# Kernel tuning notes

Measured on AMD Instinct MI355X. Metric: run time of the kernel, lower is better.

Reference implementation:

```python
import jax, jax.numpy as jnp
import numpy as np
from jax.scipy.special import logsumexp

T, B, D, L = 1024, 32, 768, 48
NEG = jnp.float32(-1e20)


def setup_inputs() -> dict:
    key = jax.random.key(0)
    ks = jax.random.split(key, 10)
    feats = jax.random.normal(ks[0], (T, B, D), jnp.float32)
    # tags: True = label disallowed at this position (partial annotation mask)
    tags = jax.random.uniform(ks[1], (T, B, L)) < 0.3
    lens = jax.random.randint(ks[2], (B,), T // 2, T + 1)
    W = jax.random.normal(ks[3], (D, L), jnp.float32) * 0.02
    b = jnp.zeros((L,), jnp.float32)
    base = jnp.float32(1.0 / L)
    begin_transition = jnp.full((L,), base) + 0.01 * jax.random.normal(ks[4], (L,), jnp.float32)
    transitions = jnp.full((L, L), base) + 0.01 * jax.random.normal(ks[5], (L, L), jnp.float32)
    end_transition = jnp.full((L,), base) + 0.01 * jax.random.normal(ks[6], (L,), jnp.float32)
    begin_constraints = jax.random.uniform(ks[7], (L,)) < 0.2
    end_constraints = jax.random.uniform(ks[8], (L,)) < 0.2
    transition_constraints = jax.random.uniform(ks[9], (L, L)) < 0.2
    return {
        "feats": feats, "tags": tags, "lens": lens,
        "W": W, "b": b,
        "begin_transition": begin_transition, "transitions": transitions,
        "end_transition": end_transition,
        "begin_constraints": begin_constraints, "end_constraints": end_constraints,
        "transition_constraints": transition_constraints,
    }


def _crf_logZ(emissions, begin, trans, end, tag_mask, lens):
    """Forward algorithm over [T,B,L] emissions; tag_mask True = disallowed.
    Returns log partition per batch element, read out at step lens-1."""
    fs0 = emissions[0] + begin[None, :]              # [B, L]
    fs0 = jnp.where(tag_mask[0], NEG, fs0)

    def step(prev, xs):
        em_t, m_t = xs
        # new[b, j] = logsumexp_k(prev[b, k] + trans[j, k]) + em_t[b, j]
        new = logsumexp(prev[:, None, :] + trans[None, :, :], axis=-1) + em_t
        new = jnp.where(m_t, NEG, new)
        return new, new

    _, ys = jax.lax.scan(step, fs0, (emissions[1:], tag_mask[1:]))
    all_fs = jnp.concatenate([fs0[None], ys], axis=0)        # [T, B, L]
    last = all_fs[lens - 1, jnp.arange(lens.shape[0])]       # [B, L]
    return logsumexp(last + end[None, :], axis=-1)           # [B]


def reference(feats, tags, lens, W, b, begin_transition, transitions,
              end_transition, begin_constraints, end_constraints,
              transition_constraints):
    # feature2labels (Dropout is identity in eval)
    emissions = jnp.einsum('tbd,dl->tbl', feats, W) + b      # [T, B, L]
    no_mask = jnp.zeros_like(tags)

    # forward_alg: unconstrained partition function
    fwd = _crf_logZ(emissions, begin_transition, transitions,
                    end_transition, no_mask, lens)

    # partial_score: constrained params + gold tag masking
    begin_m = jnp.where(begin_constraints, NEG, begin_transition)
    trans_m = jnp.where(transition_constraints, NEG, transitions)
    end_m = jnp.where(end_constraints, NEG, end_transition)
    par = _crf_logZ(emissions, begin_m, trans_m, end_m, tags, lens)

    # criterion per batch element (sum over batch = original scalar loss)
    return fwd - par                                          # [B]
```

## Files before the change

### kernel.cpp

```cpp
#include <hip/hip_runtime.h>

#define T_ 1024
#define B_ 32
#define D_ 768
#define L_ 48
#define TB_ (T_ * B_)

__global__ __launch_bounds__(256, 1) void emis_gemm(
    const float* __restrict__ feats, const float* __restrict__ W,
    const float* __restrict__ bias, float* __restrict__ E) {
  __shared__ float fbuf[128 * 64];
  __shared__ float wbuf[48 * 68];
  const int tid = threadIdx.x;
  const int wv = tid >> 6;
  const int lane = tid & 63;
  const int cg = tid & 7;
  const int rg = tid >> 3;
  const int c0 = cg * 6;
  const int rowbase = blockIdx.x * 128;
  const int r7 = rg & 7;

  float acc[4][6];
#pragma unroll
  for (int i = 0; i < 4; i++)
#pragma unroll
    for (int c = 0; c < 6; c++) acc[i][c] = 0.f;

  for (int kc = 0; kc < D_; kc += 64) {
    __syncthreads();

#pragma unroll
    for (int inst = 0; inst < 8; inst++) {
      const int rowstart = wv * 32 + inst * 4;
      const int r = rowstart + (lane >> 4);
      const int slot = lane & 15;
      const int gch = slot ^ (r & 7);
      const float* g = feats + (size_t)(rowbase + r) * D_ + kc + gch * 4;
      float* l = fbuf + rowstart * 64;
      __builtin_amdgcn_global_load_lds(
          (const __attribute__((address_space(1))) uint32_t*)g,
          (__attribute__((address_space(3))) uint32_t*)l, 16, 0, 0);
    }

#pragma unroll
    for (int i = 0; i < 12; i++) {
      const int idx = tid + i * 256;
      const int ko = idx / 48;
      const int j = idx - ko * 48;
      wbuf[j * 68 + ko] = W[(kc + ko) * L_ + j];
    }

    __syncthreads();

#pragma unroll 4
    for (int k4 = 0; k4 < 16; k4++) {
      float4 fv[4];
      float4 wv4[6];
      const int sch = (k4 ^ r7) << 2;
#pragma unroll
      for (int i = 0; i < 4; i++)
        fv[i] = *(const float4*)(fbuf + (rg + 32 * i) * 64 + sch);
#pragma unroll
      for (int c = 0; c < 6; c++)
        wv4[c] = *(const float4*)(wbuf + (c0 + c) * 68 + k4 * 4);
#pragma unroll
      for (int i = 0; i < 4; i++) {
#pragma unroll
        for (int c = 0; c < 6; c++) {
          acc[i][c] = fmaf(fv[i].x, wv4[c].x, acc[i][c]);
          acc[i][c] = fmaf(fv[i].y, wv4[c].y, acc[i][c]);
          acc[i][c] = fmaf(fv[i].z, wv4[c].z, acc[i][c]);
          acc[i][c] = fmaf(fv[i].w, wv4[c].w, acc[i][c]);
        }
      }
    }
  }

#pragma unroll
  for (int i = 0; i < 4; i++) {
    float* dst = E + (size_t)(rowbase + rg + 32 * i) * L_ + c0;
#pragma unroll
    for (int c = 0; c < 6; c += 2) {
      float2 v;
      v.x = __expf(acc[i][c + 0] + bias[c0 + c + 0]);
      v.y = __expf(acc[i][c + 1] + bias[c0 + c + 1]);
      *(float2*)(dst + c) = v;
    }
  }
}

__global__ __launch_bounds__(64, 1) void crf_scan(
    const float* __restrict__ E, const int* __restrict__ tags,
    const int* __restrict__ lens, const float* __restrict__ begin,
    const float* __restrict__ trans, const float* __restrict__ endt,
    const int* __restrict__ bc, const int* __restrict__ ec,
    const int* __restrict__ tc, float* __restrict__ out) {
  const int s = blockIdx.x;
  const int pass = s & 1;
  const int b = s >> 1;
  const int lane = threadIdx.x;
  const bool act = lane < L_;
  const int len = lens[b];
  const int stride = B_ * L_;
  const int base = b * L_ + (act ? lane : 0);

  float P[L_];
#pragma unroll
  for (int k = 0; k < L_; k++) P[k] = 0.f;
  if (act) {
#pragma unroll
    for (int k = 0; k < L_; k++) {
      float p = __expf(trans[lane * L_ + k]);
      if (pass && tc[lane * L_ + k]) p = 0.f;
      P[k] = p;
    }
  }

  float a = 0.f;
  if (act) {
    a = E[base] * __expf(begin[lane]);
    if (pass && (bc[lane] || tags[base])) a = 0.f;
  }
  float logacc = 0.f;

  auto step = [&](float ev, int tg, bool rescale) {
    const int ai = __float_as_int(a);
    int sa[L_];
#pragma unroll
    for (int k = 0; k < L_; k++) sa[k] = __builtin_amdgcn_readlane(ai, k);
    float s0 = 0.f, s1 = 0.f, s2 = 0.f, s3 = 0.f;
#pragma unroll
    for (int k = 0; k < L_; k += 4) {
      s0 = fmaf(__int_as_float(sa[k + 0]), P[k + 0], s0);
      s1 = fmaf(__int_as_float(sa[k + 1]), P[k + 1], s1);
      s2 = fmaf(__int_as_float(sa[k + 2]), P[k + 2], s2);
      s3 = fmaf(__int_as_float(sa[k + 3]), P[k + 3], s3);
    }
    float u = ((s0 + s1) + (s2 + s3)) * ev;
    if (pass && tg) u = 0.f;
    if (rescale) {
      float m = u;
#pragma unroll
      for (int off = 32; off; off >>= 1) m = fmaxf(m, __shfl_xor(m, off, 64));
      m = fmaxf(m, 1e-30f);
      u = u / m;
      logacc += __logf(m);
    }
    a = u;
  };

  float e8[8];
  int tg8[8];
#pragma unroll
  for (int i = 0; i < 8; i++) {
    e8[i] = E[(1 + i) * stride + base];
    tg8[i] = pass ? tags[(1 + i) * stride + base] : 0;
  }

  int t = 1;
  for (; t + 8 <= len; t += 8) {
    float p8[8];
    int q8[8];
#pragma unroll
    for (int i = 0; i < 8; i++) {
      int tt = t + 8 + i;
      tt = (tt < len) ? tt : (len - 1);
      p8[i] = E[tt * stride + base];
      q8[i] = pass ? tags[tt * stride + base] : 0;
    }
#pragma unroll
    for (int i = 0; i < 8; i++) step(e8[i], tg8[i], i == 7);
#pragma unroll
    for (int i = 0; i < 8; i++) { e8[i] = p8[i]; tg8[i] = q8[i]; }
  }
#pragma unroll
  for (int i = 0; i < 8; i++) {
    if (t + i < len) step(e8[i], tg8[i], false);
  }

  float z = 0.f;
  if (act) {
    float ez = __expf(endt[lane]);
    if (pass && ec[lane]) ez = 0.f;
    z = a * ez;
  }
#pragma unroll
  for (int off = 32; off; off >>= 1) z += __shfl_xor(z, off, 64);
  const float logZ = logacc + __logf(z);
  if (lane == 0) atomicAdd(out + b, pass ? -logZ : logZ);
}

extern "C" void kernel_launch(void* const* d_in, const int* in_sizes, int n_in,
                              void* d_out, int out_size, void* d_ws,
                              size_t ws_size, hipStream_t stream) {
  (void)in_sizes; (void)n_in; (void)out_size; (void)ws_size;
  const float* feats = (const float*)d_in[0];
  const int* tags = (const int*)d_in[1];
  const int* lens = (const int*)d_in[2];
  const float* W = (const float*)d_in[3];
  const float* bias = (const float*)d_in[4];
  const float* begin = (const float*)d_in[5];
  const float* trans = (const float*)d_in[6];
  const float* endt = (const float*)d_in[7];
  const int* bc = (const int*)d_in[8];
  const int* ec = (const int*)d_in[9];
  const int* tc = (const int*)d_in[10];

  float* E = (float*)d_ws;
  float* out = (float*)d_out;

  hipMemsetAsync(d_out, 0, B_ * sizeof(float), stream);

  emis_gemm<<<dim3(TB_ / 128), dim3(256), 0, stream>>>(feats, W, bias, E);
  crf_scan<<<dim3(2 * B_), dim3(64), 0, stream>>>(E, tags, lens, begin, trans,
                                                  endt, bc, ec, tc, out);
}
```

Before: 448.3 us.

## Double-buffer GEMM staging and pack CRF scan chains into multi-wave blocks

The emission GEMM now double-buffers the feature and weight tiles in shared memory, prefetching the next K-chunk while computing the current one, so there is one barrier per chunk instead of two. The CRF scan folds the tag mask into the emission value at load time, replaces the division with a hardware reciprocal, and packs eight sequence chains into each 512-thread block instead of one 64-thread block per chain. Packing chains onto fewer CUs may make the latency-bound scan waves compete for issue slots. The extra shared buffer also raises LDS use in the GEMM.

New measurement: 837.8 us. +86.9%, slower.

```diff
diff --git a/kernel.cpp b/kernel.cpp
--- a/kernel.cpp
+++ b/kernel.cpp
@@ -9,8 +9,8 @@
 __global__ __launch_bounds__(256, 1) void emis_gemm(
     const float* __restrict__ feats, const float* __restrict__ W,
     const float* __restrict__ bias, float* __restrict__ E) {
-  __shared__ float fbuf[128 * 64];
-  __shared__ float wbuf[48 * 68];
+  __shared__ float fbuf[2][128 * 64];
+  __shared__ float wbuf[2][48 * 68];
   const int tid = threadIdx.x;
   const int wv = tid >> 6;
   const int lane = tid & 63;
@@ -26,9 +26,9 @@
 #pragma unroll
     for (int c = 0; c < 6; c++) acc[i][c] = 0.f;
 
-  for (int kc = 0; kc < D_; kc += 64) {
-    __syncthreads();
-
+  float wreg[12];
+
+  auto stage_feats = [&](int kc, int bufi) {
 #pragma unroll
     for (int inst = 0; inst < 8; inst++) {
       const int rowstart = wv * 32 + inst * 4;
@@ -36,22 +36,42 @@
       const int slot = lane & 15;
       const int gch = slot ^ (r & 7);
       const float* g = feats + (size_t)(rowbase + r) * D_ + kc + gch * 4;
-      float* l = fbuf + rowstart * 64;
+      float* l = &fbuf[bufi][rowstart * 64];
       __builtin_amdgcn_global_load_lds(
           (const __attribute__((address_space(1))) uint32_t*)g,
           (__attribute__((address_space(3))) uint32_t*)l, 16, 0, 0);
     }
-
+  };
+  auto load_w = [&](int kc) {
 #pragma unroll
     for (int i = 0; i < 12; i++) {
       const int idx = tid + i * 256;
       const int ko = idx / 48;
       const int j = idx - ko * 48;
-      wbuf[j * 68 + ko] = W[(kc + ko) * L_ + j];
-    }
-
-    __syncthreads();
-
+      wreg[i] = W[(kc + ko) * L_ + j];
+    }
+  };
+  auto store_w = [&](int bufi) {
+#pragma unroll
+    for (int i = 0; i < 12; i++) {
+      const int idx = tid + i * 256;
+      const int ko = idx / 48;
+      const int j = idx - ko * 48;
+      wbuf[bufi][j * 68 + ko] = wreg[i];
+    }
+  };
+
+  stage_feats(0, 0);
+  load_w(0);
+  store_w(0);
+  __syncthreads();
+
+  for (int c = 0; c < 12; c++) {
+    const int cur = c & 1, nxt = cur ^ 1;
+    if (c + 1 < 12) {
+      stage_feats((c + 1) * 64, nxt);
+      load_w((c + 1) * 64);
+    }
 #pragma unroll 4
     for (int k4 = 0; k4 < 16; k4++) {
       float4 fv[4];
@@ -59,21 +79,23 @@
       const int sch = (k4 ^ r7) << 2;
 #pragma unroll
       for (int i = 0; i < 4; i++)
-        fv[i] = *(const float4*)(fbuf + (rg + 32 * i) * 64 + sch);
-#pragma unroll
-      for (int c = 0; c < 6; c++)
-        wv4[c] = *(const float4*)(wbuf + (c0 + c) * 68 + k4 * 4);
+        fv[i] = *(const float4*)(&fbuf[cur][(rg + 32 * i) * 64 + sch]);
+#pragma unroll
+      for (int cc = 0; cc < 6; cc++)
+        wv4[cc] = *(const float4*)(&wbuf[cur][(c0 + cc) * 68 + k4 * 4]);
 #pragma unroll
       for (int i = 0; i < 4; i++) {
 #pragma unroll
-        for (int c = 0; c < 6; c++) {
-          acc[i][c] = fmaf(fv[i].x, wv4[c].x, acc[i][c]);
-          acc[i][c] = fmaf(fv[i].y, wv4[c].y, acc[i][c]);
-          acc[i][c] = fmaf(fv[i].z, wv4[c].z, acc[i][c]);
-          acc[i][c] = fmaf(fv[i].w, wv4[c].w, acc[i][c]);
+        for (int cc = 0; cc < 6; cc++) {
+          acc[i][cc] = fmaf(fv[i].x, wv4[cc].x, acc[i][cc]);
+          acc[i][cc] = fmaf(fv[i].y, wv4[cc].y, acc[i][cc]);
+          acc[i][cc] = fmaf(fv[i].z, wv4[cc].z, acc[i][cc]);
+          acc[i][cc] = fmaf(fv[i].w, wv4[cc].w, acc[i][cc]);
         }
       }
     }
+    if (c + 1 < 12) store_w(nxt);
+    __syncthreads();
   }
 
 #pragma unroll
@@ -89,16 +111,17 @@
   }
 }
 
-__global__ __launch_bounds__(64, 1) void crf_scan(
+__global__ __launch_bounds__(512, 2) void crf_scan(
     const float* __restrict__ E, const int* __restrict__ tags,
     const int* __restrict__ lens, const float* __restrict__ begin,
     const float* __restrict__ trans, const float* __restrict__ endt,
     const int* __restrict__ bc, const int* __restrict__ ec,
     const int* __restrict__ tc, float* __restrict__ out) {
-  const int s = blockIdx.x;
+  const int wvid = threadIdx.x >> 6;
+  const int lane = threadIdx.x & 63;
+  const int s = blockIdx.x * 8 + wvid;
   const int pass = s & 1;
   const int b = s >> 1;
-  const int lane = threadIdx.x;
   const bool act = lane < L_;
   const int len = lens[b];
   const int stride = B_ * L_;
@@ -123,7 +146,13 @@
   }
   float logacc = 0.f;
 
-  auto step = [&](float ev, int tg, bool rescale) {
+  auto ldE = [&](int tt) -> float {
+    float v = E[tt * stride + base];
+    if (pass && tags[tt * stride + base]) v = 0.f;
+    return v;
+  };
+
+  auto step = [&](float ev, bool rescale) {
     const int ai = __float_as_int(a);
     int sa[L_];
 #pragma unroll
@@ -137,45 +166,38 @@
       s3 = fmaf(__int_as_float(sa[k + 3]), P[k + 3], s3);
     }
     float u = ((s0 + s1) + (s2 + s3)) * ev;
-    if (pass && tg) u = 0.f;
     if (rescale) {
       float m = u;
 #pragma unroll
       for (int off = 32; off; off >>= 1) m = fmaxf(m, __shfl_xor(m, off, 64));
       m = fmaxf(m, 1e-30f);
-      u = u / m;
+      u = u * __builtin_amdgcn_rcpf(m);
       logacc += __logf(m);
     }
     a = u;
   };
 
   float e8[8];
-  int tg8[8];
-#pragma unroll
-  for (int i = 0; i < 8; i++) {
-    e8[i] = E[(1 + i) * stride + base];
-    tg8[i] = pass ? tags[(1 + i) * stride + base] : 0;
-  }
+#pragma unroll
+  for (int i = 0; i < 8; i++) e8[i] = ldE(1 + i);
 
   int t = 1;
   for (; t + 8 <= len; t += 8) {
     float p8[8];
-    int q8[8];
 #pragma unroll
     for (int i = 0; i < 8; i++) {
       int tt = t + 8 + i;
       tt = (tt < len) ? tt : (len - 1);
-      p8[i] = E[tt * stride + base];
-      q8[i] = pass ? tags[tt * stride + base] : 0;
-    }
-#pragma unroll
-    for (int i = 0; i < 8; i++) step(e8[i], tg8[i], i == 7);
-#pragma unroll
-    for (int i = 0; i < 8; i++) { e8[i] = p8[i]; tg8[i] = q8[i]; }
+      p8[i] = ldE(tt);
+    }
+#pragma unroll
+    for (int i = 0; i < 8; i++) step(e8[i], i == 7);
+#pragma unroll
+    for (int i = 0; i < 8; i++) e8[i] = p8[i];
   }
 #pragma unroll
   for (int i = 0; i < 8; i++) {
-    if (t + i < len) step(e8[i], tg8[i], false);
+    if (t + i < len) step(e8[i], false);
   }
 
   float z = 0.f;
@@ -212,6 +234,6 @@
   hipMemsetAsync(d_out, 0, B_ * sizeof(float), stream);
 
   emis_gemm<<<dim3(TB_ / 128), dim3(256), 0, stream>>>(feats, W, bias, E);
-  crf_scan<<<dim3(2 * B_), dim3(64), 0, stream>>>(E, tags, lens, begin, trans,
-                                                  endt, bc, ec, tc, out);
+  crf_scan<<<dim3(8), dim3(512), 0, stream>>>(E, tags, lens, begin, trans,
+                                              endt, bc, ec, tc, out);
 }
```
